# Performance work log

Hardware: AMD Instinct MI355X
Metric: run time of the kernel (lower is better)

Reference implementation:

```python
import jax, jax.numpy as jnp
import numpy as np

ALPHA, BETA, GAMMA = 0.05, 0.95, 0.95   # list_weight
TANH_ALPHA = 2.0
GDEP = 2


def _gcn_rnn(x, adp, preA, W, b):
    # GCN type 'RNN': adaptive batched adj + predefined adj
    h = x
    outs = [h]
    for _ in range(GDEP):
        h = (ALPHA * x
             + BETA * jnp.einsum('nvc,nvw->nwc', h, adp)
             + GAMMA * jnp.einsum('nvc,vw->nwc', h, preA))
        outs.append(h)
    return jnp.concatenate(outs, -1) @ W + b


def _gcn_hyper(x, A, W, b):
    h = x
    outs = [h]
    for _ in range(GDEP):
        h = ALPHA * x + GAMMA * jnp.einsum('nvc,vw->nwc', h, A)
        outs.append(h)
    return jnp.concatenate(outs, -1) @ W + b


def _gcn_tgn(x, Ab, W, b):
    h = x
    outs = [h]
    for _ in range(GDEP):
        h = ALPHA * x + GAMMA * jnp.einsum('nvc,nvw->nwc', h, Ab)
        outs.append(h)
    return jnp.concatenate(outs, -1) @ W + b


def setup_inputs() -> dict:
    key = jax.random.key(0)
    ks = jax.random.split(key, 28)
    B, T, N, F = 16, 24, 512, 2
    H, E = 64, 16          # hidden_size, node embedding dim (dims_hyper[-1])
    TGN_OUT = 32
    D_ATTN = 4 * F         # TAttn default dim_out = 4 * dim_in
    p = lambda i, shape: jax.random.normal(ks[i], shape, dtype=jnp.float32) * 0.1
    return {
        'sample': jax.random.normal(ks[0], (B, T, N, F), dtype=jnp.float32),
        'predefined_A': jax.random.uniform(ks[1], (N, N), dtype=jnp.float32),
        'w_query': p(2, (F, D_ATTN)), 'w_key': p(3, (F, D_ATTN)),
        'attn_bias': p(4, (D_ATTN,)), 'attn_trans': p(5, (D_ATTN, 1)),
        'W_tgn': p(6, ((GDEP + 1) * F, TGN_OUT)), 'b_tgn': p(7, (TGN_OUT,)),
        'W_agg1': p(8, ((GDEP + 1) * H, E)), 'b_agg1': p(9, (E,)),
        'W_agg2': p(10, ((GDEP + 1) * H, E)), 'b_agg2': p(11, (E,)),
        'W_srcemb': p(12, (F, E)), 'b_srcemb': p(13, (E,)),
        'W_tgtemb': p(14, (F, E)), 'b_tgtemb': p(15, (E,)),
        'W_gz': p(16, ((GDEP + 1) * (F + H), H)), 'b_gz': p(17, (H,)),
        'W_gr': p(18, ((GDEP + 1) * (F + H), H)), 'b_gr': p(19, (H,)),
        'W_gc': p(20, ((GDEP + 1) * (F + H), H)), 'b_gc': p(21, (H,)),
        'W_short': p(22, (TGN_OUT, F)), 'b_short': p(23, (F,)),
        'W_long': p(24, (H, F)), 'b_long': p(25, (F,)),
        'W_mix': p(26, (TGN_OUT + H, F)), 'b_mix': p(27, (F,)),
    }


def reference(sample, predefined_A, w_query, w_key, attn_bias, attn_trans,
              W_tgn, b_tgn, W_agg1, b_agg1, W_agg2, b_agg2,
              W_srcemb, b_srcemb, W_tgtemb, b_tgtemb,
              W_gz, b_gz, W_gr, b_gr, W_gc, b_gc,
              W_short, b_short, W_long, b_long, W_mix, b_mix):
    B, T, N, F = sample.shape
    H = W_long.shape[0]
    A = predefined_A
    eye = jnp.eye(N, dtype=sample.dtype)

    def gru_step(hidden, graph):
        # hidden: [B,N,H], graph: [B,N,F]
        gs = _gcn_hyper(hidden, A, W_agg1, b_agg1)
        gt = _gcn_hyper(hidden, A, W_agg2, b_agg2)
        nv_s = jnp.tanh(TANH_ALPHA * (graph @ W_srcemb + b_srcemb) * gs)
        nv_t = jnp.tanh(TANH_ALPHA * (graph @ W_tgtemb + b_tgtemb) * gt)
        a = (jnp.einsum('bnd,bmd->bnm', nv_s, nv_t)
             - jnp.einsum('bnd,bmd->bnm', nv_t, nv_s))
        adp = jax.nn.relu(jnp.tanh(TANH_ALPHA * a)) + eye
        adp = adp / adp.sum(-1, keepdims=True)           # row-normalized [B,N,N]
        combined = jnp.concatenate([graph, hidden], -1)
        z = jax.nn.sigmoid(_gcn_rnn(combined, adp, A, W_gz, b_gz))
        r = jax.nn.sigmoid(_gcn_rnn(combined, adp, A, W_gr, b_gr))
        c = jnp.tanh(_gcn_rnn(jnp.concatenate([graph, r * hidden], -1), adp, A, W_gc, b_gc))
        return z * hidden + (1.0 - z) * c

    hidden = jnp.zeros((B, N, H), dtype=sample.dtype)
    graphs = jnp.moveaxis(sample[:, 0:T - 4:4], 1, 0)    # [T', B, N, F]
    hidden = jax.lax.scan(lambda h, g: (gru_step(h, g), None), hidden, graphs)[0]

    # temporal additive attention over the last 4 graphs (TAttn)
    src = sample[:, -4:]                                  # [B,4,N,F]
    tar = sample[:, -1]                                   # [B,N,F]
    q = (tar @ w_query)[:, None, :, None, :]              # [B,1,N,1,D]
    k = (src @ w_key)[:, :, None, :, :]                   # [B,4,1,N,D]
    scores = (jnp.tanh(q + k + attn_bias) @ attn_trans)[..., 0]   # [B,4,N,N]
    attn = jax.nn.softmax(scores, axis=-1)

    # single TGN layer: graph conv with (predefined + attention) adjacency
    Ab = A[None] + attn.reshape(-1, N, N)                 # [B*4,N,N]
    out = _gcn_tgn(src.reshape(-1, N, F), Ab, W_tgn, b_tgn)
    out = jax.nn.relu(out.reshape(B, 4, N, -1))
    tar = out.sum(axis=1)                                 # [B,N,TGN_OUT]

    gat_result = tar @ W_short + b_short                  # [B,N,F]
    hidden = gru_step(hidden, gat_result)
    gru_result = hidden @ W_long + b_long
    final_result = jnp.concatenate([tar, hidden], -1) @ W_mix + b_mix
    return gat_result, gru_result, final_result, attn
```

## Files before the change

kernel.cpp:

```cpp
#include <hip/hip_runtime.h>

#define ALPHA_C 0.05f
#define BETA_C  0.95f
#define GAMMA_C 0.95f

constexpr int B = 16, T = 24, N = 512, F = 2, H = 64, E = 16;
constexpr int DA = 8;
constexpr int CC = F + H;
constexpr int TGN_OC = 32;
constexpr int NPART = 4;

__device__ __forceinline__ float fast_rcp(float x) { return __builtin_amdgcn_rcpf(x); }
__device__ __forceinline__ float fast_tanh(float x) {
    return 1.0f - 2.0f * fast_rcp(__expf(2.0f * x) + 1.0f);
}
__device__ __forceinline__ float fast_sigmoid(float x) {
    return fast_rcp(1.0f + __expf(-x));
}

__global__ void scaleA_kernel(const float* __restrict__ A, float* __restrict__ K1)
{
    int i = blockIdx.x * 256 + threadIdx.x;
    K1[i] = GAMMA_C * A[i];
}

__global__ __launch_bounds__(256) void k2_kernel(const float* __restrict__ A,
                                                 float* __restrict__ K2)
{
    __shared__ float rows[16][258];
    __shared__ float cols[256][17];
    const int tid = threadIdx.x;
    const int r0 = blockIdx.y * 16, c0 = blockIdx.x * 16;
    const int rr = tid >> 4, cc = tid & 15;
    float acc = 0.f;
    for (int k0 = 0; k0 < N; k0 += 256) {
#pragma unroll
        for (int it = 0; it < 4; ++it) {
            int l = it * 256 + tid;
            int row = l >> 6, k4 = (l & 63) << 2;
            *(float4*)&rows[row][k4] = *(const float4*)(A + (size_t)(r0 + row) * N + k0 + k4);
        }
#pragma unroll
        for (int it = 0; it < 4; ++it) {
            int l = it * 256 + tid;
            int k = l >> 2, c4 = (l & 3) << 2;
            *(float4*)&cols[k][c4] = *(const float4*)(A + (size_t)(k0 + k) * N + c0 + c4);
        }
        __syncthreads();
#pragma unroll 8
        for (int k = 0; k < 256; ++k) acc += rows[rr][k] * cols[k][cc];
        __syncthreads();
    }
    size_t i = (size_t)(r0 + rr) * N + c0 + cc;
    K2[i] = GAMMA_C * ALPHA_C * A[i] + GAMMA_C * GAMMA_C * acc;
}

template<bool INSUM>
__global__ __launch_bounds__(512) void bmm4_kernel(
    float* __restrict__ out, const float* __restrict__ x, const float* __restrict__ in,
    const float* __restrict__ M)
{
    __shared__ float sh_m[128][64];
    __shared__ float sh_h[64][68];
    constexpr int Crow = CC;
    const size_t pstr = (size_t)B * N * Crow;
    const int tid = threadIdx.x;
    const int b = blockIdx.z, w0 = blockIdx.x * 64, vq = blockIdx.y;
    const int cg = tid & 15;
    const int wg = tid >> 4;

    float acc[2][4] = {{0,0,0,0},{0,0,0,0}};
    float ag[2] = {0.f, 0.f};

    const float* Mb = M + (size_t)b * N * N;
    const float* inb = in + (size_t)b * N * Crow;

#pragma unroll
    for (int it = 0; it < 4; ++it) {
        int l = it * 512 + tid;
        int row = l >> 4, c4 = (l & 15) << 2;
        *(float4*)&sh_m[row][c4] =
            *(const float4*)(Mb + (size_t)(vq * 128 + row) * N + w0 + c4);
    }

    for (int vt = 0; vt < 2; ++vt) {
        const int v0 = vq * 128 + vt * 64;
        {
            const float2* h0 = (const float2*)(inb + (size_t)v0 * Crow);
            for (int l = tid; l < 64 * 33; l += 512) {
                int row = l / 33, k = (l - row * 33) * 2;
                float2 v = h0[l];
                if (INSUM) {
#pragma unroll
                    for (int j = 1; j < NPART; ++j) {
                        float2 w = ((const float2*)(inb + (size_t)j * pstr + (size_t)v0 * Crow))[l];
                        v.x += w.x; v.y += w.y;
                    }
                }
                *(float2*)&sh_h[row][k] = v;
            }
        }
        __syncthreads();
#pragma unroll 8
        for (int j = 0; j < 64; ++j) {
            float2 mv = *(const float2*)&sh_m[vt * 64 + j][wg << 1];
            float4 hv = *(const float4*)&sh_h[j][cg << 2];
            acc[0][0] += mv.x * hv.x; acc[0][1] += mv.x * hv.y;
            acc[0][2] += mv.x * hv.z; acc[0][3] += mv.x * hv.w;
            acc[1][0] += mv.y * hv.x; acc[1][1] += mv.y * hv.y;
            acc[1][2] += mv.y * hv.z; acc[1][3] += mv.y * hv.w;
            if (cg < 2) {
                float gv = sh_h[j][64 + cg];
                ag[0] += mv.x * gv; ag[1] += mv.y * gv;
            }
        }
        if (vt == 0) __syncthreads();
    }
    float* outp = out + (size_t)vq * pstr + (size_t)b * N * Crow;
    const float* xb = x + (size_t)b * N * Crow;
#pragma unroll
    for (int r = 0; r < 2; ++r) {
        const int w = w0 + (wg << 1) + r;
        const size_t base = (size_t)w * Crow + (cg << 2);
        float o0 = acc[r][0], o1 = acc[r][1], o2 = acc[r][2], o3 = acc[r][3];
        if (vq == 0) {
            o0 += ALPHA_C * xb[base];     o1 += ALPHA_C * xb[base + 1];
            o2 += ALPHA_C * xb[base + 2]; o3 += ALPHA_C * xb[base + 3];
        }
        float2 lo = {o0, o1}, hi = {o2, o3};
        *(float2*)(outp + base) = lo;
        *(float2*)(outp + base + 2) = hi;
        if (cg < 2) {
            size_t gb = (size_t)w * Crow + 64 + cg;
            float v = ag[r];
            if (vq == 0) v += ALPHA_C * xb[gb];
            outp[gb] = v;
        }
    }
}

__global__ __launch_bounds__(512) void hyper3_kernel(
    float* __restrict__ P1, float* __restrict__ P2, const float* __restrict__ hidden,
    const float* __restrict__ K1, const float* __restrict__ K2)
{
    __shared__ float sh_m1[64][68];
    __shared__ float sh_m2[64][68];
    __shared__ float sh_h[64][68];
    const size_t pstr = (size_t)B * N * H;
    const int tid = threadIdx.x;
    const int b = blockIdx.z, w0 = blockIdx.x * 64, vq = blockIdx.y;
    const int cg = tid & 15;
    const int wg = tid >> 4;

    float a1[2][4] = {{0,0,0,0},{0,0,0,0}};
    float a2[2][4] = {{0,0,0,0},{0,0,0,0}};
    const float* inb = hidden + (size_t)b * N * H;

    for (int vt = 0; vt < 2; ++vt) {
        const int v0 = vq * 128 + vt * 64;
#pragma unroll
        for (int it = 0; it < 2; ++it) {
            int l = it * 512 + tid;
            int row = l >> 4, c4 = (l & 15) << 2;
            *(float4*)&sh_m1[row][c4] =
                *(const float4*)(K1 + (size_t)(v0 + row) * N + w0 + c4);
            *(float4*)&sh_m2[row][c4] =
                *(const float4*)(K2 + (size_t)(v0 + row) * N + w0 + c4);
            *(float4*)&sh_h[row][c4] =
                *(const float4*)(inb + (size_t)(v0 + row) * H + c4);
        }
        __syncthreads();
#pragma unroll 8
        for (int j = 0; j < 64; ++j) {
            float2 m1 = *(const float2*)&sh_m1[j][wg << 1];
            float2 m2 = *(const float2*)&sh_m2[j][wg << 1];
            float4 hv = *(const float4*)&sh_h[j][cg << 2];
            a1[0][0] += m1.x * hv.x; a1[0][1] += m1.x * hv.y;
            a1[0][2] += m1.x * hv.z; a1[0][3] += m1.x * hv.w;
            a1[1][0] += m1.y * hv.x; a1[1][1] += m1.y * hv.y;
            a1[1][2] += m1.y * hv.z; a1[1][3] += m1.y * hv.w;
            a2[0][0] += m2.x * hv.x; a2[0][1] += m2.x * hv.y;
            a2[0][2] += m2.x * hv.z; a2[0][3] += m2.x * hv.w;
            a2[1][0] += m2.y * hv.x; a2[1][1] += m2.y * hv.y;
            a2[1][2] += m2.y * hv.z; a2[1][3] += m2.y * hv.w;
        }
        __syncthreads();
    }
    float* o1 = P1 + (size_t)vq * pstr + (size_t)b * N * H;
    float* o2 = P2 + (size_t)vq * pstr + (size_t)b * N * H;
#pragma unroll
    for (int r = 0; r < 2; ++r) {
        const int w = w0 + (wg << 1) + r;
        const size_t base = (size_t)w * H + (cg << 2);
        float4 v1 = {a1[r][0], a1[r][1], a1[r][2], a1[r][3]};
        float4 v2 = {a2[r][0], a2[r][1], a2[r][2], a2[r][3]};
        if (vq == 0) {
            float4 xv = *(const float4*)(inb + base);
            v1.x += ALPHA_C * xv.x; v1.y += ALPHA_C * xv.y;
            v1.z += ALPHA_C * xv.z; v1.w += ALPHA_C * xv.w;
            v2.x += ALPHA_C * xv.x; v2.y += ALPHA_C * xv.y;
            v2.z += ALPHA_C * xv.z; v2.w += ALPHA_C * xv.w;
        }
        *(float4*)(o1 + base) = v1;
        *(float4*)(o2 + base) = v2;
    }
}

__global__ __launch_bounds__(256) void gsgt5_kernel(
    const float* __restrict__ hidden, const float* __restrict__ P1, const float* __restrict__ P2,
    const float* __restrict__ Wa1, const float* __restrict__ ba1,
    const float* __restrict__ Wa2, const float* __restrict__ ba2,
    const float* __restrict__ graph, long gstride,
    const float* __restrict__ Wsrc, const float* __restrict__ bsrc,
    const float* __restrict__ Wtgt, const float* __restrict__ btgt,
    float* __restrict__ nv_s, float* __restrict__ nv_t)
{
    constexpr size_t psH = (size_t)B * N * H;
    __shared__ float sh[16][196];
    __shared__ float W1t[16][196];
    __shared__ float W2t[16][196];
    const int tid = threadIdx.x;
    const int e = tid & 15;
    const int row = tid >> 4;
    const size_t nn0 = (size_t)blockIdx.x * 16;
    {
        int f4 = ((int)(nn0) + row) * 16 + e;
        float4 v = ((const float4*)hidden)[f4];
        *(float4*)&sh[row][e << 2] = v;
        float4 a = ((const float4*)P1)[f4];
#pragma unroll
        for (int j = 1; j < NPART; ++j) {
            float4 w = ((const float4*)(P1 + (size_t)j * psH))[f4];
            a.x += w.x; a.y += w.y; a.z += w.z; a.w += w.w;
        }
        *(float4*)&sh[row][64 + (e << 2)] = a;
        float4 c = ((const float4*)P2)[f4];
#pragma unroll
        for (int j = 1; j < NPART; ++j) {
            float4 w = ((const float4*)(P2 + (size_t)j * psH))[f4];
            c.x += w.x; c.y += w.y; c.z += w.z; c.w += w.w;
        }
        *(float4*)&sh[row][128 + (e << 2)] = c;
    }
    for (int l = tid; l < 768; l += 256) {
        int sk = l >> 2, q = l & 3;
        float4 w1 = ((const float4*)Wa1)[l];
        float4 w2 = ((const float4*)Wa2)[l];
        W1t[4 * q + 0][sk] = w1.x; W1t[4 * q + 1][sk] = w1.y;
        W1t[4 * q + 2][sk] = w1.z; W1t[4 * q + 3][sk] = w1.w;
        W2t[4 * q + 0][sk] = w2.x; W2t[4 * q + 1][sk] = w2.y;
        W2t[4 * q + 2][sk] = w2.z; W2t[4 * q + 3][sk] = w2.w;
    }
    __syncthreads();
    float gs = ba1[e], gt = ba2[e];
#pragma unroll 8
    for (int sk = 0; sk < 192; sk += 4) {
        float4 xv = *(const float4*)&sh[row][sk];
        float4 w1 = *(const float4*)&W1t[e][sk];
        float4 w2 = *(const float4*)&W2t[e][sk];
        gs += xv.x * w1.x + xv.y * w1.y + xv.z * w1.z + xv.w * w1.w;
        gt += xv.x * w2.x + xv.y * w2.y + xv.z * w2.z + xv.w * w2.w;
    }
    size_t nn = nn0 + row;
    int b = (int)(nn >> 9), n = (int)(nn & (N - 1));
    const float* g = graph + (size_t)b * gstride + (size_t)n * F;
    float g0 = g[0], g1 = g[1];
    float es = g0 * Wsrc[e] + g1 * Wsrc[E + e] + bsrc[e];
    float et = g0 * Wtgt[e] + g1 * Wtgt[E + e] + btgt[e];
    nv_s[nn * E + e] = fast_tanh(2.0f * es * gs);
    nv_t[nn * E + e] = fast_tanh(2.0f * et * gt);
}

__global__ __launch_bounds__(512) void adp3_kernel(
    const float* __restrict__ nv_s, const float* __restrict__ nv_t,
    const float* __restrict__ A,
    const float* __restrict__ hidden, const float* __restrict__ graph, long gstride,
    float* __restrict__ Mcomb, float* __restrict__ comb)
{
    __shared__ float red[8][4];
    __shared__ float tot[4];
    const int m = threadIdx.x;
    const int n0 = blockIdx.x * 4;
    const int b = blockIdx.y;
    const float4* sm = (const float4*)(nv_s + ((size_t)b * N + m) * E);
    const float4* tm = (const float4*)(nv_t + ((size_t)b * N + m) * E);
    const float4* sn = (const float4*)(nv_s + ((size_t)b * N + n0) * E);
    const float4* tn = (const float4*)(nv_t + ((size_t)b * N + n0) * E);
    float a1[4] = {0.f,0.f,0.f,0.f}, a2[4] = {0.f,0.f,0.f,0.f};
#pragma unroll
    for (int dd = 0; dd < 4; ++dd) {
        float4 smv = sm[dd], tmv = tm[dd];
#pragma unroll
        for (int r = 0; r < 4; ++r) {
            float4 snv = sn[r * 4 + dd], tnv = tn[r * 4 + dd];
            a1[r] += snv.x * tmv.x + snv.y * tmv.y + snv.z * tmv.z + snv.w * tmv.w;
            a2[r] += tnv.x * smv.x + tnv.y * smv.y + tnv.z * smv.z + tnv.w * smv.w;
        }
    }
    float p[4];
#pragma unroll
    for (int r = 0; r < 4; ++r) {
        float pv = fmaxf(fast_tanh(2.0f * (a1[r] - a2[r])), 0.0f);
        if (m == n0 + r) pv += 1.0f;
        p[r] = pv;
    }
    float sr[4] = {p[0], p[1], p[2], p[3]};
    for (int o = 32; o > 0; o >>= 1) {
#pragma unroll
        for (int r = 0; r < 4; ++r) sr[r] += __shfl_down(sr[r], o);
    }
    int wid = m >> 6, lane = m & 63;
    if (lane == 0) {
#pragma unroll
        for (int r = 0; r < 4; ++r) red[wid][r] = sr[r];
    }
    __syncthreads();
    if (m < 4) {
        float t = 0.f;
        for (int i = 0; i < 8; ++i) t += red[i][m];
        tot[m] = BETA_C * fast_rcp(t);
    }
    __syncthreads();
#pragma unroll
    for (int r = 0; r < 4; ++r)
        Mcomb[((size_t)b * N + n0 + r) * N + m] =
            GAMMA_C * A[(size_t)(n0 + r) * N + m] + p[r] * tot[r];
    if (m < 4 * CC) {
        int r = m / CC, k = m - r * CC;
        size_t nn = (size_t)b * N + n0 + r;
        float v;
        if (k < F) v = graph[(size_t)b * gstride + (size_t)(n0 + r) * F + k];
        else       v = hidden[nn * H + (k - F)];
        comb[nn * CC + k] = v;
    }
}

__device__ __forceinline__ void stage_xt(float (*Xt)[20], const float* __restrict__ base,
                                         const float* __restrict__ P1,
                                         const float* __restrict__ P2,
                                         size_t nn0, int tid)
{
    constexpr size_t psC = (size_t)B * N * CC;
    const float2* c2 = (const float2*)(base + nn0 * CC);
    const float2* p1b = (const float2*)(P1 + nn0 * CC);
    const float2* p2b = (const float2*)(P2 + nn0 * CC);
    for (int l = tid; l < 16 * 33; l += 256) {
        int row = l & 15, kp = l >> 4;
        int idx = row * 33 + kp;
        float2 v = c2[idx];
        Xt[2 * kp][row] = v.x; Xt[2 * kp + 1][row] = v.y;
        float2 a = p1b[idx];
#pragma unroll
        for (int j = 1; j < NPART; ++j) {
            float2 w = ((const float2*)(P1 + (size_t)j * psC + nn0 * CC))[idx];
            a.x += w.x; a.y += w.y;
        }
        Xt[66 + 2 * kp][row] = a.x; Xt[66 + 2 * kp + 1][row] = a.y;
        float2 c = p2b[idx];
#pragma unroll
        for (int j = 1; j < NPART; ++j) {
            float2 w = ((const float2*)(P2 + (size_t)j * psC + nn0 * CC))[idx];
            c.x += w.x; c.y += w.y;
        }
        Xt[132 + 2 * kp][row] = c.x; Xt[132 + 2 * kp + 1][row] = c.y;
    }
}

__global__ __launch_bounds__(256) void zr5_kernel(
    const float* __restrict__ comb, const float* __restrict__ P1, const float* __restrict__ P2,
    const float* __restrict__ Wgz, const float* __restrict__ bgz,
    const float* __restrict__ Wgr, const float* __restrict__ bgr,
    const float* __restrict__ hidden,
    float* __restrict__ z, float* __restrict__ comb2)
{
    __shared__ float Xt[198][20];
    __shared__ float Wl[66][128];
    const int tid = threadIdx.x;
    const size_t nn0 = (size_t)blockIdx.x * 16;

    stage_xt(Xt, comb, P1, P2, nn0, tid);

    const int cp = tid & 63;
    const int rg = tid >> 6;
    float2 bias = (cp < 32) ? *(const float2*)&bgz[2 * cp]
                            : *(const float2*)&bgr[2 * cp - 64];
    float acc[4][2];
#pragma unroll
    for (int r = 0; r < 4; ++r) { acc[r][0] = bias.x; acc[r][1] = bias.y; }

    for (int ch = 0; ch < 3; ++ch) {
        const int sk0 = ch * 66;
        for (int l = tid; l < 66 * 32; l += 256) {
            int j = l >> 5, q = l & 31;
            float4 w = (q < 16)
                ? ((const float4*)(Wgz + (size_t)(sk0 + j) * H))[q]
                : ((const float4*)(Wgr + (size_t)(sk0 + j) * H))[q - 16];
            *(float4*)&Wl[j][q << 2] = w;
        }
        __syncthreads();
#pragma unroll 6
        for (int j = 0; j < 66; ++j) {
            float4 xv = *(const float4*)&Xt[sk0 + j][rg << 2];
            float2 wv = *(const float2*)&Wl[j][cp << 1];
            acc[0][0] += xv.x * wv.x; acc[0][1] += xv.x * wv.y;
            acc[1][0] += xv.y * wv.x; acc[1][1] += xv.y * wv.y;
            acc[2][0] += xv.z * wv.x; acc[2][1] += xv.z * wv.y;
            acc[3][0] += xv.w * wv.x; acc[3][1] += xv.w * wv.y;
        }
        __syncthreads();
    }

    if (cp < 32) {
        const int oc = 2 * cp;
#pragma unroll
        for (int r = 0; r < 4; ++r) {
            size_t nn = nn0 + (rg << 2) + r;
            z[nn * H + oc]     = fast_sigmoid(acc[r][0]);
            z[nn * H + oc + 1] = fast_sigmoid(acc[r][1]);
        }
    } else {
        const int oc = 2 * cp - 64;
#pragma unroll
        for (int r = 0; r < 4; ++r) {
            size_t nn = nn0 + (rg << 2) + r;
            float h0 = hidden[nn * H + oc], h1 = hidden[nn * H + oc + 1];
            comb2[nn * CC + F + oc]     = fast_sigmoid(acc[r][0]) * h0;
            comb2[nn * CC + F + oc + 1] = fast_sigmoid(acc[r][1]) * h1;
        }
    }
    if (tid < 32) {
        int row = tid >> 1, f = tid & 1;
        comb2[(nn0 + row) * CC + f] = Xt[f][row];
    }
}

__global__ __launch_bounds__(256) void cup5_kernel(
    const float* __restrict__ comb2, const float* __restrict__ P1, const float* __restrict__ P2,
    const float* __restrict__ Wgc, const float* __restrict__ bgc,
    const float* __restrict__ z, float* __restrict__ hidden)
{
    __shared__ float Xt[198][20];
    __shared__ float Wl[66][64];
    const int tid = threadIdx.x;
    const size_t nn0 = (size_t)blockIdx.x * 16;

    stage_xt(Xt, comb2, P1, P2, nn0, tid);

    const int cp = tid & 31;
    const int rg = tid >> 5;
    float2 bias = *(const float2*)&bgc[2 * cp];
    float acc[2][2];
#pragma unroll
    for (int r = 0; r < 2; ++r) { acc[r][0] = bias.x; acc[r][1] = bias.y; }

    for (int ch = 0; ch < 3; ++ch) {
        const int sk0 = ch * 66;
        for (int l = tid; l < 66 * 16; l += 256) {
            int j = l >> 4, q = l & 15;
            float4 w = ((const float4*)(Wgc + (size_t)(sk0 + j) * H))[q];
            *(float4*)&Wl[j][q << 2] = w;
        }
        __syncthreads();
#pragma unroll 6
        for (int j = 0; j < 66; ++j) {
            float2 xv = *(const float2*)&Xt[sk0 + j][rg << 1];
            float2 wv = *(const float2*)&Wl[j][cp << 1];
            acc[0][0] += xv.x * wv.x; acc[0][1] += xv.x * wv.y;
            acc[1][0] += xv.y * wv.x; acc[1][1] += xv.y * wv.y;
        }
        __syncthreads();
    }

    const int oc = 2 * cp;
#pragma unroll
    for (int r = 0; r < 2; ++r) {
        size_t nn = nn0 + (rg << 1) + r;
        float cv0 = fast_tanh(acc[r][0]);
        float cv1 = fast_tanh(acc[r][1]);
        float zv0 = z[nn * H + oc],     ho0 = hidden[nn * H + oc];
        float zv1 = z[nn * H + oc + 1], ho1 = hidden[nn * H + oc + 1];
        hidden[nn * H + oc]     = zv0 * ho0 + (1.0f - zv0) * cv0;
        hidden[nn * H + oc + 1] = zv1 * ho1 + (1.0f - zv1) * cv1;
    }
}

__global__ void qk_kernel(const float* __restrict__ sample,
                          const float* __restrict__ wq, const float* __restrict__ wk,
                          const float* __restrict__ attn_bias,
                          float* __restrict__ q, float* __restrict__ kk)
{
    int idx = blockIdx.x * 256 + threadIdx.x;
    if (idx < B * N * DA) {
        int d = idx & 7;
        int n = (idx >> 3) & (N - 1);
        int b = idx >> 12;
        const float* tar = sample + (((size_t)b * T + (T - 1)) * N + n) * F;
        q[idx] = tar[0] * wq[d] + tar[1] * wq[DA + d] + attn_bias[d];
    } else {
        int j = idx - B * N * DA;
        int d = j & 7;
        int n = (j >> 3) & (N - 1);
        int t = (j >> 12) & 3;
        int b = j >> 14;
        const float* s = sample + (((size_t)b * T + (T - 4 + t)) * N + n) * F;
        kk[j] = s[0] * wk[d] + s[1] * wk[DA + d];
    }
}

__global__ __launch_bounds__(256) void scores3_kernel(
    const float* __restrict__ q, const float* __restrict__ kk,
    const float* __restrict__ trans, float* __restrict__ attn)
{
    int bt = blockIdx.y;
    int b = bt >> 2;
    int rbase = blockIdx.x * 16;
    int wid = threadIdx.x >> 6, lane = threadIdx.x & 63;
    const float* kkbt = kk + (size_t)bt * N * DA;
    float* attnbt = attn + (size_t)bt * N * N;
    float tr[8];
#pragma unroll
    for (int d = 0; d < 8; ++d) tr[d] = trans[d];
    for (int i = 0; i < 4; ++i) {
        int n = rbase + wid * 4 + i;
        const float* qp = q + ((size_t)b * N + n) * DA;
        float4 qa = *(const float4*)qp, qb = *(const float4*)(qp + 4);
        float ev[8]; float ssum = 0.f;
#pragma unroll
        for (int k = 0; k < 8; ++k) {
            const float* kp = kkbt + (size_t)(k * 64 + lane) * DA;
            float4 ka = *(const float4*)kp, kb = *(const float4*)(kp + 4);
            float s = fast_tanh(qa.x + ka.x) * tr[0] + fast_tanh(qa.y + ka.y) * tr[1]
                    + fast_tanh(qa.z + ka.z) * tr[2] + fast_tanh(qa.w + ka.w) * tr[3]
                    + fast_tanh(qb.x + kb.x) * tr[4] + fast_tanh(qb.y + kb.y) * tr[5]
                    + fast_tanh(qb.z + kb.z) * tr[6] + fast_tanh(qb.w + kb.w) * tr[7];
            ev[k] = __expf(s);
            ssum += ev[k];
        }
        for (int o = 32; o > 0; o >>= 1) ssum += __shfl_down(ssum, o);
        ssum = __shfl(ssum, 0);
        float rinv = fast_rcp(ssum);
#pragma unroll
        for (int k = 0; k < 8; ++k)
            attnbt[(size_t)n * N + k * 64 + lane] = ev[k] * rinv;
    }
}

__global__ __launch_bounds__(256) void tgn2_kernel(
    const float* __restrict__ A, const float* __restrict__ attn,
    const float* __restrict__ hbase, long hsB, long hsT,
    const float* __restrict__ xbase, long xsB, long xsT,
    float* __restrict__ out)
{
    __shared__ float sh_m[64][65];
    __shared__ float sh_h[64][2];
    int bt = blockIdx.y;
    int w0 = blockIdx.x * 64;
    int tid = threadIdx.x;
    int wl = tid >> 2, c = tid & 1, vh = (tid >> 1) & 1;
    const float* hp = hbase + (size_t)(bt >> 2) * hsB + (size_t)(bt & 3) * hsT;
    const float* ap = attn + (size_t)bt * N * N;
    float acc = 0.f;
    for (int vt = 0; vt < 8; ++vt) {
        int v0 = vt * 64;
#pragma unroll
        for (int it = 0; it < 16; ++it) {
            int l = it * 256 + tid;
            int vr = l >> 6, wc = l & 63;
            size_t gi = (size_t)(v0 + vr) * N + (w0 + wc);
            sh_m[wc][vr] = A[gi] + ap[gi];
        }
        if (tid < 128) sh_h[tid >> 1][tid & 1] = hp[(size_t)(v0 + (tid >> 1)) * F + (tid & 1)];
        __syncthreads();
#pragma unroll
        for (int jj = 0; jj < 32; ++jj) {
            int j = vh * 32 + jj;
            acc += sh_m[wl][j] * sh_h[j][c];
        }
        __syncthreads();
    }
    acc += __shfl_xor(acc, 2);
    if (vh == 0) {
        const float* xp = xbase + (size_t)(bt >> 2) * xsB + (size_t)(bt & 3) * xsT;
        out[((size_t)bt * N + w0 + wl) * F + c] =
            ALPHA_C * xp[(size_t)(w0 + wl) * F + c] + GAMMA_C * acc;
    }
}

__global__ __launch_bounds__(256) void tgn_out_gat_kernel(
    const float* __restrict__ sample,
    const float* __restrict__ th1, const float* __restrict__ th2,
    const float* __restrict__ Wt, const float* __restrict__ bt_,
    const float* __restrict__ Ws, const float* __restrict__ bs,
    float* __restrict__ tar32, float* __restrict__ out0)
{
    __shared__ float sh_t[8][33];
    const int tid = threadIdx.x;
    const int oc = tid & 31;
    const int r = tid >> 5;
    const size_t nn = (size_t)blockIdx.x * 8 + r;
    const int n = (int)(nn & (N - 1));
    const int b = (int)(nn >> 9);
    float acc = 0.f;
    for (int t = 0; t < 4; ++t) {
        int bt = b * 4 + t;
        const float* s = sample + (((size_t)b * T + (T - 4 + t)) * N + n) * F;
        size_t rr = ((size_t)bt * N + n) * F;
        float v = bt_[oc];
        v += s[0] * Wt[0 * TGN_OC + oc] + s[1] * Wt[1 * TGN_OC + oc];
        v += th1[rr] * Wt[2 * TGN_OC + oc] + th1[rr + 1] * Wt[3 * TGN_OC + oc];
        v += th2[rr] * Wt[4 * TGN_OC + oc] + th2[rr + 1] * Wt[5 * TGN_OC + oc];
        acc += fmaxf(v, 0.0f);
    }
    tar32[nn * TGN_OC + oc] = acc;
    sh_t[r][oc] = acc;
    __syncthreads();
    if (tid < 16) {
        int row = tid >> 1, f = tid & 1;
        size_t nn2 = (size_t)blockIdx.x * 8 + row;
        float g = bs[f];
#pragma unroll
        for (int k = 0; k < TGN_OC; ++k) g += sh_t[row][k] * Ws[(size_t)k * F + f];
        out0[nn2 * F + f] = g;
    }
}

__global__ void final_kernel(const float* __restrict__ hidden, const float* __restrict__ tar32,
                             const float* __restrict__ Wl, const float* __restrict__ bl,
                             const float* __restrict__ Wm, const float* __restrict__ bm,
                             float* __restrict__ dout_gru, float* __restrict__ dout_fin)
{
    int idx = blockIdx.x * 256 + threadIdx.x;
    int f = idx & 1;
    int nn = idx >> 1;
    const float* hp = hidden + (size_t)nn * H;
    const float* tp = tar32 + (size_t)nn * TGN_OC;
    float g = bl[f], fin = bm[f];
    for (int k = 0; k < H; ++k) g += hp[k] * Wl[(size_t)k * F + f];
    for (int k = 0; k < TGN_OC; ++k) fin += tp[k] * Wm[(size_t)k * F + f];
    for (int k = 0; k < H; ++k) fin += hp[k] * Wm[(size_t)(TGN_OC + k) * F + f];
    dout_gru[idx] = g;
    dout_fin[idx] = fin;
}

namespace {
struct Ptrs {
    const float *sample, *A, *wq, *wk, *attn_bias, *attn_trans, *Wt, *bt_;
    const float *Wa1, *ba1, *Wa2, *ba2, *Wsrc, *bsrc, *Wtgt, *btgt;
    const float *Wgz, *bgz, *Wgr, *bgr, *Wgc, *bgc, *Wsh, *bsh, *Wl, *bl, *Wm, *bm;
    float *hidden, *nvs, *nvt, *Mcomb, *K1, *K2, *comb, *comb2, *z, *P1, *P2;
    float *q, *kk, *th1, *th2, *tar32;
};

void gru_step(hipStream_t stream, const Ptrs& p, const float* graph, long gstride)
{
    dim3 bg(8, NPART, B);
    hyper3_kernel<<<bg, 512, 0, stream>>>(p.P1, p.P2, p.hidden, p.K1, p.K2);
    gsgt5_kernel<<<B * N / 16, 256, 0, stream>>>(
        p.hidden, p.P1, p.P2, p.Wa1, p.ba1, p.Wa2, p.ba2, graph, gstride,
        p.Wsrc, p.bsrc, p.Wtgt, p.btgt, p.nvs, p.nvt);
    adp3_kernel<<<dim3(N / 4, B), 512, 0, stream>>>(
        p.nvs, p.nvt, p.A, p.hidden, graph, gstride, p.Mcomb, p.comb);
    bmm4_kernel<false><<<bg, 512, 0, stream>>>(p.P1, p.comb, p.comb, p.Mcomb);
    bmm4_kernel<true><<<bg, 512, 0, stream>>>(p.P2, p.comb, p.P1, p.Mcomb);
    zr5_kernel<<<B * N / 16, 256, 0, stream>>>(
        p.comb, p.P1, p.P2, p.Wgz, p.bgz, p.Wgr, p.bgr, p.hidden, p.z, p.comb2);
    bmm4_kernel<false><<<bg, 512, 0, stream>>>(p.P1, p.comb2, p.comb2, p.Mcomb);
    bmm4_kernel<true><<<bg, 512, 0, stream>>>(p.P2, p.comb2, p.P1, p.Mcomb);
    cup5_kernel<<<B * N / 16, 256, 0, stream>>>(
        p.comb2, p.P1, p.P2, p.Wgc, p.bgc, p.z, p.hidden);
}
}

extern "C" void kernel_launch(void* const* d_in, const int* in_sizes, int n_in,
                              void* d_out, int out_size, void* d_ws, size_t ws_size,
                              hipStream_t stream)
{
    (void)in_sizes; (void)n_in; (void)out_size; (void)ws_size;
    Ptrs p;
    p.sample = (const float*)d_in[0];
    p.A      = (const float*)d_in[1];
    p.wq     = (const float*)d_in[2];
    p.wk     = (const float*)d_in[3];
    p.attn_bias  = (const float*)d_in[4];
    p.attn_trans = (const float*)d_in[5];
    p.Wt  = (const float*)d_in[6];
    p.bt_ = (const float*)d_in[7];
    p.Wa1 = (const float*)d_in[8];
    p.ba1 = (const float*)d_in[9];
    p.Wa2 = (const float*)d_in[10];
    p.ba2 = (const float*)d_in[11];
    p.Wsrc = (const float*)d_in[12];
    p.bsrc = (const float*)d_in[13];
    p.Wtgt = (const float*)d_in[14];
    p.btgt = (const float*)d_in[15];
    p.Wgz = (const float*)d_in[16];
    p.bgz = (const float*)d_in[17];
    p.Wgr = (const float*)d_in[18];
    p.bgr = (const float*)d_in[19];
    p.Wgc = (const float*)d_in[20];
    p.bgc = (const float*)d_in[21];
    p.Wsh = (const float*)d_in[22];
    p.bsh = (const float*)d_in[23];
    p.Wl  = (const float*)d_in[24];
    p.bl  = (const float*)d_in[25];
    p.Wm  = (const float*)d_in[26];
    p.bm  = (const float*)d_in[27];

    float* ws = (float*)d_ws;
    size_t off = 0;
    auto alloc = [&](size_t nelem) { float* r = ws + off; off += nelem; return r; };
    p.hidden = alloc((size_t)B * N * H);
    p.nvs    = alloc((size_t)B * N * E);
    p.nvt    = alloc((size_t)B * N * E);
    p.Mcomb  = alloc((size_t)B * N * N);
    p.K1     = alloc((size_t)N * N);
    p.K2     = alloc((size_t)N * N);
    p.comb   = alloc((size_t)B * N * CC);
    p.comb2  = alloc((size_t)B * N * CC);
    p.z      = alloc((size_t)B * N * H);
    p.P1     = alloc((size_t)NPART * B * N * CC);
    p.P2     = alloc((size_t)NPART * B * N * CC);
    p.q      = alloc((size_t)B * N * DA);
    p.kk     = alloc((size_t)B * 4 * N * DA);
    p.th1    = alloc((size_t)B * 4 * N * F);
    p.th2    = alloc((size_t)B * 4 * N * F);
    p.tar32  = alloc((size_t)B * N * TGN_OC);

    float* out = (float*)d_out;
    float* out_gat = out;
    float* out_gru = out + (size_t)B * N * F;
    float* out_fin = out + (size_t)2 * B * N * F;
    float* out_attn = out + (size_t)3 * B * N * F;

    hipMemsetAsync(p.hidden, 0, (size_t)B * N * H * sizeof(float), stream);
    scaleA_kernel<<<N * N / 256, 256, 0, stream>>>(p.A, p.K1);
    k2_kernel<<<dim3(32, 32), 256, 0, stream>>>(p.A, p.K2);

    for (int i = 0; i < 5; ++i) {
        const float* graph = p.sample + (size_t)(4 * i) * N * F;
        gru_step(stream, p, graph, (long)T * N * F);
    }

    qk_kernel<<<(B * N * DA + B * 4 * N * DA) / 256, 256, 0, stream>>>(
        p.sample, p.wq, p.wk, p.attn_bias, p.q, p.kk);
    scores3_kernel<<<dim3(32, 64), 256, 0, stream>>>(p.q, p.kk, p.attn_trans, out_attn);

    const float* srcbase = p.sample + (size_t)(T - 4) * N * F;
    tgn2_kernel<<<dim3(8, 64), 256, 0, stream>>>(
        p.A, out_attn, srcbase, (long)T * N * F, (long)N * F,
        srcbase, (long)T * N * F, (long)N * F, p.th1);
    tgn2_kernel<<<dim3(8, 64), 256, 0, stream>>>(
        p.A, out_attn, p.th1, (long)4 * N * F, (long)N * F,
        srcbase, (long)T * N * F, (long)N * F, p.th2);
    tgn_out_gat_kernel<<<B * N / 8, 256, 0, stream>>>(
        p.sample, p.th1, p.th2, p.Wt, p.bt_, p.Wsh, p.bsh, p.tar32, out_gat);

    gru_step(stream, p, out_gat, (long)N * F);

    final_kernel<<<(B * N * F) / 256, 256, 0, stream>>>(
        p.hidden, p.tar32, p.Wl, p.bl, p.Wm, p.bm, out_gru, out_fin);
}
```

Before: 1.267 ms.

## Restructure bmm4 with split-K 4x4 register tiles and separate graph-column blocks

Result: slower. 1.337 ms (+5.6%).

```diff
diff --git a/kernel.cpp b/kernel.cpp
--- a/kernel.cpp
+++ b/kernel.cpp
@@ -60,81 +60,114 @@
     float* __restrict__ out, const float* __restrict__ x, const float* __restrict__ in,
     const float* __restrict__ M)
 {
-    __shared__ float sh_m[128][64];
-    __shared__ float sh_h[64][68];
     constexpr int Crow = CC;
     const size_t pstr = (size_t)B * N * Crow;
     const int tid = threadIdx.x;
-    const int b = blockIdx.z, w0 = blockIdx.x * 64, vq = blockIdx.y;
-    const int cg = tid & 15;
-    const int wg = tid >> 4;
-
-    float acc[2][4] = {{0,0,0,0},{0,0,0,0}};
-    float ag[2] = {0.f, 0.f};
-
-    const float* Mb = M + (size_t)b * N * N;
+    const int b = blockIdx.z, w0 = blockIdx.x * 64;
+    const int vq = blockIdx.y;
+
     const float* inb = in + (size_t)b * N * Crow;
-
+    const float* xb = x + (size_t)b * N * Crow;
+
+    if (vq == 4) {
+        const int w = w0 + (tid & 63);
+        const int sel = tid >> 6;
+        const int q = sel & 3, f = sel >> 2;
+        const float* Mb = M + (size_t)b * N * N;
+        const float* gcol = inb + 64 + f;
+        float acc = 0.f;
+#pragma unroll 4
+        for (int j = 0; j < 128; ++j) {
+            int v = q * 128 + j;
+            float g = gcol[(size_t)v * Crow];
+            if (INSUM) {
+                g += gcol[pstr + (size_t)v * Crow];
+                g += gcol[2 * pstr + (size_t)v * Crow];
+                g += gcol[3 * pstr + (size_t)v * Crow];
+            }
+            acc += Mb[(size_t)v * N + w] * g;
+        }
+        if (q == 0) acc += ALPHA_C * xb[(size_t)w * Crow + 64 + f];
+        out[(size_t)q * pstr + (size_t)b * N * Crow + (size_t)w * Crow + 64 + f] = acc;
+        return;
+    }
+
+    __shared__ float sh_m[128][64];
+    __shared__ float sh_h[128][64];
+    const int kt = tid >> 8;
+    const int sub = tid & 255;
+    const int cg = sub & 15;
+    const int wg = sub >> 4;
+
+    const float* Mb = M + (size_t)b * N * N + (size_t)vq * 128 * N + w0;
 #pragma unroll
     for (int it = 0; it < 4; ++it) {
         int l = it * 512 + tid;
         int row = l >> 4, c4 = (l & 15) << 2;
-        *(float4*)&sh_m[row][c4] =
-            *(const float4*)(Mb + (size_t)(vq * 128 + row) * N + w0 + c4);
-    }
-
-    for (int vt = 0; vt < 2; ++vt) {
-        const int v0 = vq * 128 + vt * 64;
-        {
-            const float2* h0 = (const float2*)(inb + (size_t)v0 * Crow);
-            for (int l = tid; l < 64 * 33; l += 512) {
-                int row = l / 33, k = (l - row * 33) * 2;
-                float2 v = h0[l];
-                if (INSUM) {
-#pragma unroll
-                    for (int j = 1; j < NPART; ++j) {
-                        float2 w = ((const float2*)(inb + (size_t)j * pstr + (size_t)v0 * Crow))[l];
-                        v.x += w.x; v.y += w.y;
-                    }
-                }
-                *(float2*)&sh_h[row][k] = v;
+        *(float4*)&sh_m[row][c4] = *(const float4*)(Mb + (size_t)row * N + c4);
+    }
+    {
+        const float* h0 = inb + (size_t)(vq * 128) * Crow;
+#pragma unroll
+        for (int it = 0; it < 8; ++it) {
+            int l = it * 512 + tid;
+            int row = l >> 5, k = (l & 31) << 1;
+            const float* src = h0 + (size_t)row * Crow + k;
+            float2 v = *(const float2*)src;
+            if (INSUM) {
+                float2 w1 = *(const float2*)(src + pstr);
+                float2 w2 = *(const float2*)(src + 2 * pstr);
+                float2 w3 = *(const float2*)(src + 3 * pstr);
+                v.x += w1.x + w2.x + w3.x;
+                v.y += w1.y + w2.y + w3.y;
             }
-        }
-        __syncthreads();
+            *(float2*)&sh_h[row][k] = v;
+        }
+    }
+    __syncthreads();
+
+    float acc[4][4] = {{0,0,0,0},{0,0,0,0},{0,0,0,0},{0,0,0,0}};
+    const int jb = kt * 64;
 #pragma unroll 8
-        for (int j = 0; j < 64; ++j) {
-            float2 mv = *(const float2*)&sh_m[vt * 64 + j][wg << 1];
-            float4 hv = *(const float4*)&sh_h[j][cg << 2];
-            acc[0][0] += mv.x * hv.x; acc[0][1] += mv.x * hv.y;
-            acc[0][2] += mv.x * hv.z; acc[0][3] += mv.x * hv.w;
-            acc[1][0] += mv.y * hv.x; acc[1][1] += mv.y * hv.y;
-            acc[1][2] += mv.y * hv.z; acc[1][3] += mv.y * hv.w;
-            if (cg < 2) {
-                float gv = sh_h[j][64 + cg];
-                ag[0] += mv.x * gv; ag[1] += mv.y * gv;
+    for (int j = 0; j < 64; ++j) {
+        float4 mv = *(const float4*)&sh_m[jb + j][wg << 2];
+        float4 hv = *(const float4*)&sh_h[jb + j][cg << 2];
+        acc[0][0] += mv.x * hv.x; acc[0][1] += mv.x * hv.y;
+        acc[0][2] += mv.x * hv.z; acc[0][3] += mv.x * hv.w;
+        acc[1][0] += mv.y * hv.x; acc[1][1] += mv.y * hv.y;
+        acc[1][2] += mv.y * hv.z; acc[1][3] += mv.y * hv.w;
+        acc[2][0] += mv.z * hv.x; acc[2][1] += mv.z * hv.y;
+        acc[2][2] += mv.z * hv.z; acc[2][3] += mv.z * hv.w;
+        acc[3][0] += mv.w * hv.x; acc[3][1] += mv.w * hv.y;
+        acc[3][2] += mv.w * hv.z; acc[3][3] += mv.w * hv.w;
+    }
+    __syncthreads();
+
+    float* red = &sh_m[0][0];
+    if (kt == 1) {
+#pragma unroll
+        for (int r = 0; r < 4; ++r) {
+            float4 v = {acc[r][0], acc[r][1], acc[r][2], acc[r][3]};
+            *(float4*)&red[sub * 20 + r * 4] = v;
+        }
+    }
+    __syncthreads();
+    if (kt == 0) {
+        float* outp = out + (size_t)vq * pstr + (size_t)b * N * Crow;
+#pragma unroll
+        for (int r = 0; r < 4; ++r) {
+            float4 o = *(const float4*)&red[sub * 20 + r * 4];
+            float o0 = acc[r][0] + o.x, o1 = acc[r][1] + o.y;
+            float o2 = acc[r][2] + o.z, o3 = acc[r][3] + o.w;
+            const int w = w0 + (wg << 2) + r;
+            const size_t base = (size_t)w * Crow + (cg << 2);
+            if (vq == 0) {
+                o0 += ALPHA_C * xb[base];     o1 += ALPHA_C * xb[base + 1];
+                o2 += ALPHA_C * xb[base + 2]; o3 += ALPHA_C * xb[base + 3];
             }
-        }
-        if (vt == 0) __syncthreads();
-    }
-    float* outp = out + (size_t)vq * pstr + (size_t)b * N * Crow;
-    const float* xb = x + (size_t)b * N * Crow;
-#pragma unroll
-    for (int r = 0; r < 2; ++r) {
-        const int w = w0 + (wg << 1) + r;
-        const size_t base = (size_t)w * Crow + (cg << 2);
-        float o0 = acc[r][0], o1 = acc[r][1], o2 = acc[r][2], o3 = acc[r][3];
-        if (vq == 0) {
-            o0 += ALPHA_C * xb[base];     o1 += ALPHA_C * xb[base + 1];
-            o2 += ALPHA_C * xb[base + 2]; o3 += ALPHA_C * xb[base + 3];
-        }
-        float2 lo = {o0, o1}, hi = {o2, o3};
-        *(float2*)(outp + base) = lo;
-        *(float2*)(outp + base + 2) = hi;
-        if (cg < 2) {
-            size_t gb = (size_t)w * Crow + 64 + cg;
-            float v = ag[r];
-            if (vq == 0) v += ALPHA_C * xb[gb];
-            outp[gb] = v;
+            float2 lo = {o0, o1}, hi = {o2, o3};
+            *(float2*)(outp + base) = lo;
+            *(float2*)(outp + base + 2) = hi;
         }
     }
 }
@@ -653,19 +686,20 @@
 
 void gru_step(hipStream_t stream, const Ptrs& p, const float* graph, long gstride)
 {
-    dim3 bg(8, NPART, B);
-    hyper3_kernel<<<bg, 512, 0, stream>>>(p.P1, p.P2, p.hidden, p.K1, p.K2);
+    dim3 bh(8, NPART, B);
+    dim3 bgm(8, NPART + 1, B);
+    hyper3_kernel<<<bh, 512, 0, stream>>>(p.P1, p.P2, p.hidden, p.K1, p.K2);
     gsgt5_kernel<<<B * N / 16, 256, 0, stream>>>(
         p.hidden, p.P1, p.P2, p.Wa1, p.ba1, p.Wa2, p.ba2, graph, gstride,
         p.Wsrc, p.bsrc, p.Wtgt, p.btgt, p.nvs, p.nvt);
     adp3_kernel<<<dim3(N / 4, B), 512, 0, stream>>>(
         p.nvs, p.nvt, p.A, p.hidden, graph, gstride, p.Mcomb, p.comb);
-    bmm4_kernel<false><<<bg, 512, 0, stream>>>(p.P1, p.comb, p.comb, p.Mcomb);
-    bmm4_kernel<true><<<bg, 512, 0, stream>>>(p.P2, p.comb, p.P1, p.Mcomb);
+    bmm4_kernel<false><<<bgm, 512, 0, stream>>>(p.P1, p.comb, p.comb, p.Mcomb);
+    bmm4_kernel<true><<<bgm, 512, 0, stream>>>(p.P2, p.comb, p.P1, p.Mcomb);
     zr5_kernel<<<B * N / 16, 256, 0, stream>>>(
         p.comb, p.P1, p.P2, p.Wgz, p.bgz, p.Wgr, p.bgr, p.hidden, p.z, p.comb2);
-    bmm4_kernel<false><<<bg, 512, 0, stream>>>(p.P1, p.comb2, p.comb2, p.Mcomb);
-    bmm4_kernel<true><<<bg, 512, 0, stream>>>(p.P2, p.comb2, p.P1, p.Mcomb);
+    bmm4_kernel<false><<<bgm, 512, 0, stream>>>(p.P1, p.comb2, p.comb2, p.Mcomb);
+    bmm4_kernel<true><<<bgm, 512, 0, stream>>>(p.P2, p.comb2, p.P1, p.Mcomb);
     cup5_kernel<<<B * N / 16, 256, 0, stream>>>(
         p.comb2, p.P1, p.P2, p.Wgc, p.bgc, p.z, p.hidden);
 }
```
